# Kernel tuning notes

Hardware: AMD Instinct MI355X
Metric: run time of the kernel (lower is better)

The kernel has to match this reference:

```python
import jax, jax.numpy as jnp
import numpy as np

SPATIAL_SCALE = 0.25
INV = int(1.0 / SPATIAL_SCALE)  # kernel_size == stride == 4


def _downsample_flow(flows, conv_w):
    # Fixed-weight strided conv: per-channel sum over INVxINV window * scale^3
    return jax.lax.conv_general_dilated(
        flows, conv_w, window_strides=(INV, INV), padding='VALID',
        dimension_numbers=('NCHW', 'OIHW', 'NCHW'))


def _warp_one(feat, flow):
    # feat: [C,H,W]; flow: [2,H,W] (x-displacement, y-displacement)
    C, H, W = feat.shape
    gx = jnp.arange(W, dtype=flow.dtype)[None, :] + flow[0]  # [H,W]
    gy = jnp.arange(H, dtype=flow.dtype)[:, None] + flow[1]  # [H,W]
    x0 = jnp.floor(gx)
    y0 = jnp.floor(gy)
    wx = gx - x0
    wy = gy - y0
    x0i = x0.astype(jnp.int32); x1i = x0i + 1
    y0i = y0.astype(jnp.int32); y1i = y0i + 1
    feat_flat = feat.reshape(C, H * W)

    def corner(xi, yi, w):
        valid = (xi >= 0) & (xi < W) & (yi >= 0) & (yi < H)
        idx = jnp.clip(yi, 0, H - 1) * W + jnp.clip(xi, 0, W - 1)  # [H,W]
        g = jnp.take(feat_flat, idx.reshape(-1), axis=1).reshape(C, H, W)
        return g * (w * valid.astype(w.dtype))[None, :, :]

    return (corner(x0i, y0i, (1 - wx) * (1 - wy))
            + corner(x1i, y0i, wx * (1 - wy))
            + corner(x0i, y1i, (1 - wx) * wy)
            + corner(x1i, y1i, wx * wy))


def setup_inputs() -> dict:
    key = jax.random.key(0)
    k1, k2 = jax.random.split(key)
    features = jax.random.normal(k1, (8, 256, 128, 128), dtype=jnp.float32)
    # flows at full resolution; scale so displacements span several pixels
    flows = jax.random.normal(k2, (8, 2, 512, 512), dtype=jnp.float32) * 8.0
    # fixed conv weights: diagonal entries = spatial_scale**3 (as in torch init)
    conv_w = jnp.zeros((2, 2, INV, INV), dtype=jnp.float32)
    conv_w = conv_w.at[0, 0].set(SPATIAL_SCALE ** 3).at[1, 1].set(SPATIAL_SCALE ** 3)
    return {'features': features, 'flows': flows, 'conv_w': conv_w}


def reference(features, flows, conv_w):
    f = _downsample_flow(flows, conv_w)  # [B,2,h,w] matching features
    return jax.vmap(_warp_one)(features, f)
```

## Files before the change

### kernel.cpp

```cpp
#include <hip/hip_runtime.h>

#define B   8
#define C   256
#define H   128
#define W   128
#define HW  (H * W)
#define FH  512
#define FW  512

#define TR     16
#define SLOTS  24
#define HALO   3
#define CG     16
#define RGN    (H / TR)
#define CGN    (C / CG)
#define NT     512

struct __attribute__((packed, aligned(4))) pf2 { float x, y; };
typedef float f32x2v __attribute__((ext_vector_type(2)));

__global__ __launch_bounds__(256) void downsample_kernel(
    const float* __restrict__ flows,
    const float* __restrict__ conv_w,
    float* __restrict__ f)
{
    int idx = blockIdx.x * blockDim.x + threadIdx.x;
    if (idx >= B * 2 * H * W) return;
    int x = idx & (W - 1);
    int y = (idx >> 7) & (H - 1);
    int o = (idx >> 14) & 1;
    int b = idx >> 15;

    const float* fb = flows + (size_t)b * 2 * FH * FW;
    const float* cw = conv_w + o * 2 * 16;

    float acc = 0.f;
#pragma unroll
    for (int i = 0; i < 2; ++i) {
        const float* fi = fb + (size_t)i * FH * FW;
#pragma unroll
        for (int kh = 0; kh < 4; ++kh) {
            const float4 v = *reinterpret_cast<const float4*>(
                fi + (size_t)(4 * y + kh) * FW + 4 * x);
            const float* w = cw + i * 16 + kh * 4;
            acc += v.x * w[0] + v.y * w[1] + v.z * w[2] + v.w * w[3];
        }
    }
    f[idx] = acc;
}

#define GLOAD_LDS(gsrc, ldst)                                                 \
    __builtin_amdgcn_global_load_lds(                                         \
        (const __attribute__((address_space(1))) void*)(gsrc),                \
        (__attribute__((address_space(3))) void*)(ldst), 16, 0, 0)

__global__ __launch_bounds__(NT, 6) void warp_kernel(
    const float* __restrict__ feat,
    const float* __restrict__ f,
    float* __restrict__ out)
{
    __shared__ __align__(16) float rows[2][2][SLOTS * W];

    const int hw_bid = blockIdx.x;
    const int lin = (hw_bid & 7) * 128 + (hw_bid >> 3);
    const int rg = lin & (RGN - 1);
    const int cg = (lin >> 3) & (CGN - 1);
    const int b  = lin >> 7;

    const int tid  = threadIdx.x;
    const int lane = tid & 63;
    const int wv   = tid >> 6;
    const int wq   = wv & 3;
    const int half = wv >> 2;

    const int ybase = rg * TR;
    const int row0  = ybase - HALO;
    const int pixbase = ybase * W;

    const float* featb = feat + ((size_t)b * C + (size_t)cg * CG) * HW;
    float*       outc  = out  + ((size_t)b * C + (size_t)cg * CG) * HW + pixbase;
    const float* fx_p  = f + (size_t)(b * 2 + 0) * HW;
    const float* fy_p  = f + (size_t)(b * 2 + 1) * HW;

    int goffs0, goffs1, goffs2;
    {
        const int wc0 = wq * 3 + 0, wc1 = wq * 3 + 1, wc2 = wq * 3 + 2;
        const int r0c = min(max(row0 + 2 * wc0 + (lane >> 5), 0), H - 1);
        const int r1c = min(max(row0 + 2 * wc1 + (lane >> 5), 0), H - 1);
        const int r2c = min(max(row0 + 2 * wc2 + (lane >> 5), 0), H - 1);
        goffs0 = r0c * W + (lane & 31) * 4;
        goffs1 = r1c * W + (lane & 31) * 4;
        goffs2 = r2c * W + (lane & 31) * 4;
    }

#define PREF2(s, chA) do {                                                    \
        const float* _cb = featb + (size_t)((chA) + half) * HW;               \
        float* _pl = &rows[(s)][half][0];                                     \
        GLOAD_LDS(_cb + goffs0, _pl + (wq * 3 + 0) * 256);                    \
        GLOAD_LDS(_cb + goffs1, _pl + (wq * 3 + 1) * 256);                    \
        GLOAD_LDS(_cb + goffs2, _pl + (wq * 3 + 2) * 256);                    \
    } while (0)

    PREF2(0, 0);

#define PXOF(k) (((k) >> 1) * 1024 + 2 * tid + ((k) & 1))

#define PXDECL(k) int i0_##k, i1_##k; float w0_##k, w1_##k, w2_##k, w3_##k;
    PXDECL(0) PXDECL(1) PXDECL(2) PXDECL(3)

#define WCOMP(k) do {                                                         \
        const int px  = PXOF(k);                                              \
        const int gpx = pixbase + px;                                         \
        const int x = gpx & (W - 1);                                          \
        const int y = gpx >> 7;                                               \
        const float gx = (float)x + fx_p[gpx];                                \
        const float gy = (float)y + fy_p[gpx];                                \
        const float x0f = floorf(gx);                                         \
        const float y0f = floorf(gy);                                         \
        const float wx = gx - x0f;                                            \
        const float wy = gy - y0f;                                            \
        const int x0 = (int)x0f, y0 = (int)y0f;                               \
        const int y1 = y0 + 1;                                                \
        const float u0 = 1.f - wx, u1 = wx;                                   \
        float A, Bv;                                                          \
        if (x0 >= 0 && x0 <= W - 2)      { A = u0;  Bv = u1;  }               \
        else if (x0 == W - 1)            { A = 0.f; Bv = u0;  }               \
        else if (x0 == -1)               { A = u1;  Bv = 0.f; }               \
        else                             { A = 0.f; Bv = 0.f; }               \
        const int bx = min(max(x0, 0), W - 2);                                \
        const float vy0 = (y0 >= 0 && y0 < H) ? 1.f : 0.f;                    \
        const float vy1 = (y1 >= 0 && y1 < H) ? 1.f : 0.f;                    \
        const int cy0 = min(max(y0, 0), H - 1);                               \
        const int cy1 = min(max(y1, 0), H - 1);                               \
        const int s0 = cy0 - row0;                                            \
        const int s1 = cy1 - row0;                                            \
        const bool ok = (s0 >= 0) && (s1 < SLOTS);                            \
        const int cs0 = min(max(s0, 0), SLOTS - 1);                           \
        const int cs1 = min(max(s1, 0), SLOTS - 1);                           \
        i0_##k = (cs0 * W + bx) | (ok ? 0 : (int)0x80000000);                 \
        i1_##k = cs1 * W + bx;                                                \
        const float wy0 = (1.f - wy) * vy0;                                   \
        const float wy1 = wy * vy1;                                           \
        w0_##k = A * wy0;  w1_##k = Bv * wy0;                                 \
        w2_##k = A * wy1;  w3_##k = Bv * wy1;                                 \
    } while (0)

    WCOMP(0); WCOMP(1); WCOMP(2); WCOMP(3);

    const int anybad = ((i0_0 | i0_1 | i0_2 | i0_3) < 0);

    asm volatile("s_waitcnt vmcnt(0)" ::: "memory");
    __builtin_amdgcn_sched_barrier(0);
    __syncthreads();

#define FQUAD(j, k0, k1, rbA, rbB, ocA, ocB) do {                             \
        const int pxe = (j) * 1024 + 2 * tid;                                 \
        const pf2 a0 = *reinterpret_cast<const pf2*>(&rbA[i0_##k0]);          \
        const pf2 a1 = *reinterpret_cast<const pf2*>(&rbA[i1_##k0]);          \
        const pf2 c0 = *reinterpret_cast<const pf2*>(&rbA[i0_##k1]);          \
        const pf2 c1 = *reinterpret_cast<const pf2*>(&rbA[i1_##k1]);          \
        const pf2 d0 = *reinterpret_cast<const pf2*>(&rbB[i0_##k0]);          \
        const pf2 d1 = *reinterpret_cast<const pf2*>(&rbB[i1_##k0]);          \
        const pf2 e0 = *reinterpret_cast<const pf2*>(&rbB[i0_##k1]);          \
        const pf2 e1 = *reinterpret_cast<const pf2*>(&rbB[i1_##k1]);          \
        f32x2v vA, vB;                                                        \
        vA.x = a0.x * w0_##k0 + a0.y * w1_##k0 + a1.x * w2_##k0 + a1.y * w3_##k0; \
        vA.y = c0.x * w0_##k1 + c0.y * w1_##k1 + c1.x * w2_##k1 + c1.y * w3_##k1; \
        vB.x = d0.x * w0_##k0 + d0.y * w1_##k0 + d1.x * w2_##k0 + d1.y * w3_##k0; \
        vB.y = e0.x * w0_##k1 + e0.y * w1_##k1 + e1.x * w2_##k1 + e1.y * w3_##k1; \
        __builtin_nontemporal_store(vA, reinterpret_cast<f32x2v*>(ocA + pxe));\
        __builtin_nontemporal_store(vB, reinterpret_cast<f32x2v*>(ocB + pxe));\
    } while (0)

#define SPX2(k, ocA, ocB, chA) do {                                           \
        const int px = PXOF(k);                                               \
        const int gpx = pixbase + px;                                         \
        const int x = gpx & (W - 1);                                          \
        const int y = gpx >> 7;                                               \
        const int x0 = (int)floorf((float)x + fx_p[gpx]);                     \
        const int y0 = (int)floorf((float)y + fy_p[gpx]);                     \
        const int bx  = min(max(x0, 0), W - 2);                               \
        const int cy0 = min(max(y0, 0), H - 1);                               \
        const int cy1 = min(max(y0 + 1, 0), H - 1);                           \
        const float* fA = featb + (size_t)(chA) * HW;                         \
        const float* fB = fA + HW;                                            \
        ocA[px] = fA[cy0 * W + bx]     * w0_##k + fA[cy0 * W + bx + 1] * w1_##k\
                + fA[cy1 * W + bx]     * w2_##k + fA[cy1 * W + bx + 1] * w3_##k;\
        ocB[px] = fB[cy0 * W + bx]     * w0_##k + fB[cy0 * W + bx + 1] * w1_##k\
                + fB[cy1 * W + bx]     * w2_##k + fB[cy1 * W + bx + 1] * w3_##k;\
    } while (0)

    for (int p = 0; p < CG / 2; ++p) {
        const int chA = 2 * p;
        if (p < CG / 2 - 1) PREF2((p + 1) & 1, chA + 2);

        const float* rbA = &rows[p & 1][0][0];
        const float* rbB = &rows[p & 1][1][0];
        float* ocA = outc + (size_t)chA * HW;
        float* ocB = ocA + HW;
        if (__builtin_expect(anybad, 0)) {
            SPX2(0, ocA, ocB, chA); SPX2(1, ocA, ocB, chA);
            SPX2(2, ocA, ocB, chA); SPX2(3, ocA, ocB, chA);
        } else {
            FQUAD(0, 0, 1, rbA, rbB, ocA, ocB);
            FQUAD(1, 2, 3, rbA, rbB, ocA, ocB);
        }

        if (p < CG / 2 - 1) {
            asm volatile("s_waitcnt vmcnt(4)" ::: "memory");
            __builtin_amdgcn_sched_barrier(0);
            __syncthreads();
        }
    }
#undef PREF2
#undef PXDECL
#undef PXOF
#undef WCOMP
#undef FQUAD
#undef SPX2
}

extern "C" void kernel_launch(void* const* d_in, const int* in_sizes, int n_in,
                              void* d_out, int out_size, void* d_ws, size_t ws_size,
                              hipStream_t stream)
{
    const float* features = (const float*)d_in[0];
    const float* flows    = (const float*)d_in[1];
    const float* conv_w   = (const float*)d_in[2];
    float*       out      = (float*)d_out;
    float*       f        = (float*)d_ws;

    downsample_kernel<<<1024, 256, 0, stream>>>(flows, conv_w, f);
    warp_kernel<<<1024, NT, 0, stream>>>(features, f, out);
}
```

Measured before the change: 51.31 us.

## Fuse flow downsampling into warp kernel and drop separate launch

Removes the standalone downsample kernel and computes the strided-conv flow value inline per pixel inside the warp kernel, reading full-resolution flows directly. This eliminates a kernel launch and the write/read of the intermediate downsampled flow buffer. In exchange, each of the 16 channel-group blocks covering the same rows recomputes the same flow values, multiplying flow reads (mostly hitting cache) and adding ALU and register pressure in the warp kernel.

```diff
diff --git a/kernel.cpp b/kernel.cpp
--- a/kernel.cpp
+++ b/kernel.cpp
@@ -19,34 +19,28 @@
 struct __attribute__((packed, aligned(4))) pf2 { float x, y; };
 typedef float f32x2v __attribute__((ext_vector_type(2)));
 
-__global__ __launch_bounds__(256) void downsample_kernel(
-    const float* __restrict__ flows,
-    const float* __restrict__ conv_w,
-    float* __restrict__ f)
+__device__ __forceinline__ void flow_at(
+    const float* __restrict__ flows, const float* __restrict__ cw,
+    int bb, int x, int y, float& fx, float& fy)
 {
-    int idx = blockIdx.x * blockDim.x + threadIdx.x;
-    if (idx >= B * 2 * H * W) return;
-    int x = idx & (W - 1);
-    int y = (idx >> 7) & (H - 1);
-    int o = (idx >> 14) & 1;
-    int b = idx >> 15;
-
-    const float* fb = flows + (size_t)b * 2 * FH * FW;
-    const float* cw = conv_w + o * 2 * 16;
-
-    float acc = 0.f;
+    const float* p0 = flows + ((size_t)bb * 2 + 0) * FH * FW
+                    + (size_t)(4 * y) * FW + 4 * x;
+    const float* p1 = p0 + (size_t)FH * FW;
+    float ax = 0.f, ay = 0.f;
 #pragma unroll
-    for (int i = 0; i < 2; ++i) {
-        const float* fi = fb + (size_t)i * FH * FW;
-#pragma unroll
-        for (int kh = 0; kh < 4; ++kh) {
-            const float4 v = *reinterpret_cast<const float4*>(
-                fi + (size_t)(4 * y + kh) * FW + 4 * x);
-            const float* w = cw + i * 16 + kh * 4;
-            acc += v.x * w[0] + v.y * w[1] + v.z * w[2] + v.w * w[3];
-        }
+    for (int kh = 0; kh < 4; ++kh) {
+        const float4 v0 = *reinterpret_cast<const float4*>(p0 + kh * FW);
+        const float4 v1 = *reinterpret_cast<const float4*>(p1 + kh * FW);
+        const float* w00 = cw + 0 * 16 + kh * 4;
+        const float* w01 = cw + 1 * 16 + kh * 4;
+        const float* w10 = cw + 2 * 16 + kh * 4;
+        const float* w11 = cw + 3 * 16 + kh * 4;
+        ax += v0.x * w00[0] + v0.y * w00[1] + v0.z * w00[2] + v0.w * w00[3]
+            + v1.x * w01[0] + v1.y * w01[1] + v1.z * w01[2] + v1.w * w01[3];
+        ay += v0.x * w10[0] + v0.y * w10[1] + v0.z * w10[2] + v0.w * w10[3]
+            + v1.x * w11[0] + v1.y * w11[1] + v1.z * w11[2] + v1.w * w11[3];
     }
-    f[idx] = acc;
+    fx = ax; fy = ay;
 }
 
 #define GLOAD_LDS(gsrc, ldst)                                                 \
@@ -56,7 +50,8 @@
 
 __global__ __launch_bounds__(NT, 6) void warp_kernel(
     const float* __restrict__ feat,
-    const float* __restrict__ f,
+    const float* __restrict__ flows,
+    const float* __restrict__ conv_w,
     float* __restrict__ out)
 {
     __shared__ __align__(16) float rows[2][2][SLOTS * W];
@@ -79,8 +74,6 @@
 
     const float* featb = feat + ((size_t)b * C + (size_t)cg * CG) * HW;
     float*       outc  = out  + ((size_t)b * C + (size_t)cg * CG) * HW + pixbase;
-    const float* fx_p  = f + (size_t)(b * 2 + 0) * HW;
-    const float* fy_p  = f + (size_t)(b * 2 + 1) * HW;
 
     int goffs0, goffs1, goffs2;
     {
@@ -113,8 +106,10 @@
         const int gpx = pixbase + px;                                         \
         const int x = gpx & (W - 1);                                          \
         const int y = gpx >> 7;                                               \
-        const float gx = (float)x + fx_p[gpx];                                \
-        const float gy = (float)y + fy_p[gpx];                                \
+        float fxv, fyv;                                                       \
+        flow_at(flows, conv_w, b, x, y, fxv, fyv);                            \
+        const float gx = (float)x + fxv;                                      \
+        const float gy = (float)y + fyv;                                      \
         const float x0f = floorf(gx);                                         \
         const float y0f = floorf(gy);                                         \
         const float wx = gx - x0f;                                            \
@@ -177,8 +172,10 @@
         const int gpx = pixbase + px;                                         \
         const int x = gpx & (W - 1);                                          \
         const int y = gpx >> 7;                                               \
-        const int x0 = (int)floorf((float)x + fx_p[gpx]);                     \
-        const int y0 = (int)floorf((float)y + fy_p[gpx]);                     \
+        float fxv, fyv;                                                       \
+        flow_at(flows, conv_w, b, x, y, fxv, fyv);                            \
+        const int x0 = (int)floorf((float)x + fxv);                           \
+        const int y0 = (int)floorf((float)y + fyv);                           \
         const int bx  = min(max(x0, 0), W - 2);                               \
         const int cy0 = min(max(y0, 0), H - 1);                               \
         const int cy1 = min(max(y0 + 1, 0), H - 1);                           \
@@ -228,8 +225,6 @@
     const float* flows    = (const float*)d_in[1];
     const float* conv_w   = (const float*)d_in[2];
     float*       out      = (float*)d_out;
-    float*       f        = (float*)d_ws;
-
-    downsample_kernel<<<1024, 256, 0, stream>>>(flows, conv_w, f);
-    warp_kernel<<<1024, NT, 0, stream>>>(features, f, out);
+
+    warp_kernel<<<1024, NT, 0, stream>>>(features, flows, conv_w, out);
 }
```

Result: slower. 143.0 us (+178.7%).
